# Optimization experiments

Hardware: AMD Instinct MI355X
Metric: run time of the kernel (lower is better)

Reference implementation:

```python
import jax, jax.numpy as jnp
import numpy as np

K_SEM = 5          # max_semantic_edges
THRESH = 0.2       # semantic_threshold
NEG_INF = -1e30


def setup_inputs() -> dict:
    key = jax.random.key(0)
    k1, k2 = jax.random.split(key)
    message_embeddings = jax.random.normal(k1, (8192, 256), dtype=jnp.float32)
    edge_emb_table = jax.random.normal(k2, (2, 64), dtype=jnp.float32)
    return {"message_embeddings": message_embeddings, "edge_emb_table": edge_emb_table}


def reference(message_embeddings, edge_emb_table):
    N = message_embeddings.shape[0]

    # ---- temporal edges: for each i -> [i,i+1] then [i+1,i] (interleaved) ----
    i = jnp.arange(N - 1)
    fwd = jnp.stack([i, i + 1])            # [2, N-1]
    bwd = jnp.stack([i + 1, i])            # [2, N-1]
    temporal = jnp.stack([fwd, bwd], axis=2).reshape(2, -1)   # [2, 2(N-1)]
    n_temporal = 2 * (N - 1)

    # ---- semantic edges: per-row top-k over sim[i, :i] with threshold ----
    norm = jnp.sqrt(jnp.sum(message_embeddings * message_embeddings, axis=1, keepdims=True))
    emb_n = message_embeddings / jnp.maximum(norm, 1e-12)     # F.normalize(p=2)
    sim = emb_n @ emb_n.T                                      # [N, N]

    r = jnp.arange(N)[:, None]
    c = jnp.arange(N)[None, :]
    # zero out diagonal and adjacent (temporal) pairs, as the torch mask does
    sim = sim * (jnp.abs(r - c) > 1)
    # restrict candidates to j < i (strictly earlier messages)
    cand = jnp.where(c < r, sim, NEG_INF)                      # [N, N]

    vals, idxs = jax.lax.top_k(cand, K_SEM)                    # [N, K]
    sem_src = idxs.reshape(-1)                                 # [N*K]
    sem_dst = jnp.repeat(jnp.arange(N), K_SEM)                 # [N*K]
    sem_valid = (vals > THRESH).reshape(-1)                    # [N*K]

    # ---- assemble padded fixed-size edge set ----
    edge_index = jnp.concatenate([temporal, jnp.stack([sem_src, sem_dst])], axis=1)
    edge_types = jnp.concatenate(
        [jnp.zeros((n_temporal,), jnp.int32), jnp.ones((N * K_SEM,), jnp.int32)])
    valid = jnp.concatenate([jnp.ones((n_temporal,), bool), sem_valid])

    edge_attr = edge_emb_table[edge_types] * valid[:, None].astype(edge_emb_table.dtype)
    edge_index = jnp.where(valid[None, :], edge_index, -1)
    return edge_index, edge_attr, valid
```

## Files before the change

kernel.cpp:

```cpp
#include <hip/hip_runtime.h>

#define N_MSG 8192
#define DIM 256
#define KS 5
#define THRESH 0.2f
#define QSCALE 192.0f
#define FILT_I 6672
#define N_TEMPORAL (2*(N_MSG-1))
#define N_EDGES (N_TEMPORAL + N_MSG*KS)
#define ATTR_OFF (2*N_EDGES)
#define VALID_OFF (ATTR_OFF + N_EDGES*64)
#define BM 128
#define NTILE (N_MSG / BM)
#define NBLOCKS (NTILE*(NTILE+1)/2)
#define CAP 32

typedef int i32x4 __attribute__((ext_vector_type(4)));

__device__ __forceinline__ void ins5(float v, int j, float (&vv)[KS], int (&xx)[KS]) {
    float cv = v; int cj = j;
#pragma unroll
    for (int k = 0; k < KS; ++k) {
        bool b = (cv > vv[k]) || (cv == vv[k] && cj < xx[k]);
        float tv = b ? vv[k] : cv; int tj = b ? xx[k] : cj;
        vv[k] = b ? cv : vv[k];    xx[k] = b ? cj : xx[k];
        cv = tv; cj = tj;
    }
}

__global__ void normalize_k(const float* __restrict__ emb, float* __restrict__ embn,
                            unsigned int* __restrict__ embqT, int* __restrict__ cnt) {
    int lane = threadIdx.x & 63;
    int row = blockIdx.x * 4 + (threadIdx.x >> 6);
    const float4 x = *(const float4*)(emb + (size_t)row * DIM + lane * 4);
    float ss = x.x * x.x;
    ss = fmaf(x.y, x.y, ss); ss = fmaf(x.z, x.z, ss); ss = fmaf(x.w, x.w, ss);
#pragma unroll
    for (int off = 1; off <= 32; off <<= 1) ss += __shfl_xor(ss, off);
    float nrm = fmaxf(sqrtf(ss), 1e-12f);
    float4 y; y.x = x.x / nrm; y.y = x.y / nrm; y.z = x.z / nrm; y.w = x.w / nrm;
    *(float4*)(embn + (size_t)row * DIM + lane * 4) = y;
    int q0 = (int)rintf(fminf(fmaxf(y.x * QSCALE, -127.f), 127.f));
    int q1 = (int)rintf(fminf(fmaxf(y.y * QSCALE, -127.f), 127.f));
    int q2 = (int)rintf(fminf(fmaxf(y.z * QSCALE, -127.f), 127.f));
    int q3 = (int)rintf(fminf(fmaxf(y.w * QSCALE, -127.f), 127.f));
    unsigned int packed =
        (q0 & 255) | ((q1 & 255) << 8) | ((q2 & 255) << 16) | ((q3 & 255) << 24);
    embqT[(((size_t)(lane >> 2) * N_MSG + row) << 2) | (lane & 3)] = packed;
    if (lane == 0) cnt[row] = 0;
}

__global__ __launch_bounds__(256, 4)
void sim_filter_k(const i32x4* __restrict__ T, int* __restrict__ cnt,
                  int* __restrict__ cidx) {
    int t = blockIdx.x;
    int bi = (int)((sqrtf(8.0f * (float)t + 1.0f) - 1.0f) * 0.5f);
    while ((bi + 1) * (bi + 2) / 2 <= t) ++bi;
    while (bi * (bi + 1) / 2 > t) --bi;
    int bj = t - bi * (bi + 1) / 2;
    const int i0 = bi * BM, j0 = bj * BM;

    const int tid = threadIdx.x;
    const int lane = tid & 63;
    const int ws = tid >> 6;
    const int wm = ws >> 1, wn = ws & 1;
    const int lr = lane & 15, kb = lane >> 4;

    i32x4 acc[4][4];
#pragma unroll
    for (int m = 0; m < 4; ++m)
#pragma unroll
        for (int n = 0; n < 4; ++n) { i32x4 z = {0, 0, 0, 0}; acc[m][n] = z; }

#pragma unroll
    for (int kc = 0; kc < 4; ++kc) {
        const i32x4* Tc = T + (size_t)(kc * 4 + kb) * N_MSG;
        i32x4 a[4], b[4];
#pragma unroll
        for (int f = 0; f < 4; ++f) {
            a[f] = Tc[i0 + wm * 64 + f * 16 + lr];
            b[f] = Tc[j0 + wn * 64 + f * 16 + lr];
        }
#pragma unroll
        for (int m = 0; m < 4; ++m)
#pragma unroll
            for (int n = 0; n < 4; ++n)
                acc[m][n] = __builtin_amdgcn_mfma_i32_16x16x64_i8(a[m], b[n], acc[m][n], 0, 0, 0);
    }

#pragma unroll
    for (int m = 0; m < 4; ++m) {
        int i = i0 + wm * 64 + m * 16 + kb * 4;
#pragma unroll
        for (int n = 0; n < 4; ++n) {
            int j = j0 + wn * 64 + n * 16 + lr;
#pragma unroll
            for (int r = 0; r < 4; ++r) {
                int v = acc[m][n][r];
                int ii = i + r;
                if (v > FILT_I && j <= ii - 2) {
                    int c = atomicAdd(&cnt[ii], 1);
                    if (c < CAP) cidx[(size_t)ii * CAP + c] = j;
                }
            }
        }
    }
}

template<bool FUSE>
__global__ void rescue_k(const float* __restrict__ embn, const int* __restrict__ cnt,
                         const int* __restrict__ cidx, const float* __restrict__ table,
                         float* __restrict__ out) {
    int lane = threadIdx.x & 63;
    int i = blockIdx.x * 4 + (threadIdx.x >> 6);
    int nc = cnt[i]; if (nc > CAP) nc = CAP;

    float fv[KS]; int fx[KS];
#pragma unroll
    for (int k = 0; k < KS; ++k) { fv[k] = -1e30f; fx[k] = -1; }

    if (nc > 0) {
        const float4 a = *(const float4*)(embn + (size_t)i * DIM + lane * 4);
        for (int c = 0; c < nc; ++c) {
            int j = cidx[(size_t)i * CAP + c];
            const float4 b = *(const float4*)(embn + (size_t)j * DIM + lane * 4);
            float p = a.x * b.x;
            p = fmaf(a.y, b.y, p); p = fmaf(a.z, b.z, p); p = fmaf(a.w, b.w, p);
#pragma unroll
            for (int off = 1; off <= 32; off <<= 1) p += __shfl_xor(p, off);
            if (p > THRESH) ins5(p, j, fv, fx);
        }
    }
    int vcnt = 0;
#pragma unroll
    for (int k = 0; k < KS; ++k) vcnt += (fv[k] > THRESH) ? 1 : 0;

    float tsem = FUSE ? table[64 + lane] : 0.0f;
#pragma unroll
    for (int k = 0; k < KS; ++k) {
        int e = N_TEMPORAL + i * KS + k;
        bool val = (k < vcnt);
        if (lane == 0) {
            out[e]             = val ? (float)fx[k] : -1.0f;
            out[N_EDGES + e]   = val ? (float)i     : -1.0f;
            out[VALID_OFF + e] = val ? 1.0f : 0.0f;
        }
        if (FUSE) out[ATTR_OFF + (size_t)e * 64 + lane] = val ? tsem : 0.0f;
    }
    if (FUSE) {
        if (i < N_MSG - 1) {
            float ttem = table[lane];
            int e0 = 2 * i;
            out[ATTR_OFF + (size_t)e0 * 64 + lane]       = ttem;
            out[ATTR_OFF + (size_t)(e0 + 1) * 64 + lane] = ttem;
            if (lane == 0) {
                out[e0]                 = (float)i;
                out[N_EDGES + e0]       = (float)(i + 1);
                out[VALID_OFF + e0]     = 1.0f;
                out[e0 + 1]             = (float)(i + 1);
                out[N_EDGES + e0 + 1]   = (float)i;
                out[VALID_OFF + e0 + 1] = 1.0f;
            }
        }
    }
}

__global__ void attr_out_k(const float* __restrict__ table, float* __restrict__ out) {
    int idx = blockIdx.x * 256 + threadIdx.x;
    int e = idx >> 4, sub = idx & 15;
    if (e >= N_EDGES) return;
    float4 a4;
    if (e < N_TEMPORAL) {
        a4 = *(const float4*)(table + sub * 4);
        if (sub == 0) {
            int i = e >> 1;
            out[e]             = (e & 1) ? (float)(i + 1) : (float)i;
            out[N_EDGES + e]   = (e & 1) ? (float)i       : (float)(i + 1);
            out[VALID_OFF + e] = 1.0f;
        }
    } else {
        float vld = out[VALID_OFF + e];
        a4 = *(const float4*)(table + 64 + sub * 4);
        a4.x *= vld; a4.y *= vld; a4.z *= vld; a4.w *= vld;
    }
    *(float4*)(out + ATTR_OFF + (size_t)e * 64 + sub * 4) = a4;
}

extern "C" void kernel_launch(void* const* d_in, const int* in_sizes, int n_in,
                              void* d_out, int out_size, void* d_ws, size_t ws_size,
                              hipStream_t stream) {
    const float* emb   = (const float*)d_in[0];
    const float* table = (const float*)d_in[1];
    float* out = (float*)d_out;

    size_t embn_f  = (size_t)N_MSG * DIM;
    size_t embq_f  = (size_t)N_MSG * DIM / 4;
    size_t cidx_f  = (size_t)N_MSG * CAP;
    size_t cnt_f   = N_MSG;
    size_t need_bytes = (embn_f + embq_f + cidx_f + cnt_f) * 4;

    bool have_ws = (ws_size >= need_bytes);
    float* scratch = have_ws ? (float*)d_ws
                             : out + ATTR_OFF;
    float*        embn  = scratch;
    unsigned int* embqT = (unsigned int*)(scratch + embn_f);
    int*          cidx  = (int*)(scratch + embn_f + embq_f);
    int*          cnt   = (int*)(scratch + embn_f + embq_f + cidx_f);

    normalize_k<<<N_MSG / 4, 256, 0, stream>>>(emb, embn, embqT, cnt);
    sim_filter_k<<<NBLOCKS, 256, 0, stream>>>((const i32x4*)embqT, cnt, cidx);
    if (have_ws) {
        rescue_k<true><<<N_MSG / 4, 256, 0, stream>>>(embn, cnt, cidx, table, out);
    } else {
        rescue_k<false><<<N_MSG / 4, 256, 0, stream>>>(embn, cnt, cidx, table, out);
        attr_out_k<<<((size_t)N_EDGES * 16 + 255) / 256, 256, 0, stream>>>(table, out);
    }
}
```

Measured before the change: 62.83 us.

## Fuse three stages into one persistent kernel with software grid barriers

Replaces the normalize, int8 similarity filter and rescue launches with a single persistent kernel of 768 blocks. The stages are separated by atomic-counter grid barriers, which removes launch gaps between them. The MFMA loop also double-buffers its K-chunk register loads so loads overlap compute. The cost is a memset launch, barrier spin time, and a deadlock risk if all 768 blocks cannot be co-resident.

After: 196.6 us. +212.9%, slower.

```diff
diff --git a/kernel.cpp b/kernel.cpp
--- a/kernel.cpp
+++ b/kernel.cpp
@@ -14,6 +14,7 @@
 #define NTILE (N_MSG / BM)
 #define NBLOCKS (NTILE*(NTILE+1)/2)
 #define CAP 32
+#define GRID_F 768
 
 typedef int i32x4 __attribute__((ext_vector_type(4)));
 
@@ -25,6 +26,177 @@
         float tv = b ? vv[k] : cv; int tj = b ? xx[k] : cj;
         vv[k] = b ? cv : vv[k];    xx[k] = b ? cj : xx[k];
         cv = tv; cj = tj;
+    }
+}
+
+__device__ __forceinline__ void grid_bar(int* bars, int which) {
+    __syncthreads();
+    if (threadIdx.x == 0) {
+        int* base = bars + which * 128;
+        __threadfence();
+        atomicAdd(base + (blockIdx.x & 7) * 16, 1);
+        int s;
+        do {
+            s = 0;
+#pragma unroll
+            for (int q = 0; q < 8; ++q)
+                s += __hip_atomic_load(base + q * 16, __ATOMIC_RELAXED,
+                                       __HIP_MEMORY_SCOPE_AGENT);
+            if (s < GRID_F) __builtin_amdgcn_s_sleep(2);
+        } while (s < GRID_F);
+        __threadfence();
+    }
+    __syncthreads();
+}
+
+__global__ __launch_bounds__(256, 3)
+void fused_k(const float* __restrict__ emb, const float* __restrict__ table,
+             float* __restrict__ out, float* __restrict__ embn,
+             unsigned int* __restrict__ embqT, int* __restrict__ cnt,
+             int* __restrict__ cidx, int* __restrict__ gbar) {
+    const int tid = threadIdx.x;
+    const int bid = blockIdx.x;
+    const int lane = tid & 63;
+    const int wv = tid >> 6;
+
+    for (int g = bid; g < N_MSG / 4; g += GRID_F) {
+        int row = g * 4 + wv;
+        const float4 x = *(const float4*)(emb + (size_t)row * DIM + lane * 4);
+        float ss = x.x * x.x;
+        ss = fmaf(x.y, x.y, ss); ss = fmaf(x.z, x.z, ss); ss = fmaf(x.w, x.w, ss);
+#pragma unroll
+        for (int off = 1; off <= 32; off <<= 1) ss += __shfl_xor(ss, off);
+        float nrm = fmaxf(sqrtf(ss), 1e-12f);
+        float4 y; y.x = x.x / nrm; y.y = x.y / nrm; y.z = x.z / nrm; y.w = x.w / nrm;
+        *(float4*)(embn + (size_t)row * DIM + lane * 4) = y;
+        int q0 = (int)rintf(fminf(fmaxf(y.x * QSCALE, -127.f), 127.f));
+        int q1 = (int)rintf(fminf(fmaxf(y.y * QSCALE, -127.f), 127.f));
+        int q2 = (int)rintf(fminf(fmaxf(y.z * QSCALE, -127.f), 127.f));
+        int q3 = (int)rintf(fminf(fmaxf(y.w * QSCALE, -127.f), 127.f));
+        unsigned int packed =
+            (q0 & 255) | ((q1 & 255) << 8) | ((q2 & 255) << 16) | ((q3 & 255) << 24);
+        embqT[(((size_t)(lane >> 2) * N_MSG + row) << 2) | (lane & 3)] = packed;
+        if (lane == 0) cnt[row] = 0;
+    }
+    grid_bar(gbar, 0);
+
+    {
+        const i32x4* T = (const i32x4*)embqT;
+        const int ws = tid >> 6;
+        const int wm = ws >> 1, wn = ws & 1;
+        const int lr = lane & 15, kb = lane >> 4;
+
+        for (int t = bid; t < NBLOCKS; t += GRID_F) {
+            int bi = (int)((sqrtf(8.0f * (float)t + 1.0f) - 1.0f) * 0.5f);
+            while ((bi + 1) * (bi + 2) / 2 <= t) ++bi;
+            while (bi * (bi + 1) / 2 > t) --bi;
+            int bj = t - bi * (bi + 1) / 2;
+            const int i0 = bi * BM, j0 = bj * BM;
+
+            i32x4 acc[4][4];
+#pragma unroll
+            for (int m = 0; m < 4; ++m)
+#pragma unroll
+                for (int n = 0; n < 4; ++n) { i32x4 z = {0, 0, 0, 0}; acc[m][n] = z; }
+
+            auto LD = [&](int kc, i32x4* a, i32x4* b) {
+                const i32x4* Tc = T + (size_t)((kc << 2) + kb) * N_MSG;
+#pragma unroll
+                for (int f = 0; f < 4; ++f) {
+                    a[f] = Tc[i0 + wm * 64 + f * 16 + lr];
+                    b[f] = Tc[j0 + wn * 64 + f * 16 + lr];
+                }
+            };
+            auto COMP = [&](i32x4* a, i32x4* b) {
+#pragma unroll
+                for (int m = 0; m < 4; ++m)
+#pragma unroll
+                    for (int n = 0; n < 4; ++n)
+                        acc[m][n] = __builtin_amdgcn_mfma_i32_16x16x64_i8(
+                            a[m], b[n], acc[m][n], 0, 0, 0);
+            };
+
+            i32x4 a0[4], b0[4], a1[4], b1[4];
+            LD(0, a0, b0);
+            LD(1, a1, b1);
+            COMP(a0, b0);
+            LD(2, a0, b0);
+            COMP(a1, b1);
+            LD(3, a1, b1);
+            COMP(a0, b0);
+            COMP(a1, b1);
+
+#pragma unroll
+            for (int m = 0; m < 4; ++m) {
+                int i = i0 + wm * 64 + m * 16 + kb * 4;
+#pragma unroll
+                for (int n = 0; n < 4; ++n) {
+                    int j = j0 + wn * 64 + n * 16 + lr;
+#pragma unroll
+                    for (int r = 0; r < 4; ++r) {
+                        int v = acc[m][n][r];
+                        int ii = i + r;
+                        if (v > FILT_I && j <= ii - 2) {
+                            int c = atomicAdd(&cnt[ii], 1);
+                            if (c < CAP) cidx[(size_t)ii * CAP + c] = j;
+                        }
+                    }
+                }
+            }
+        }
+    }
+    grid_bar(gbar, 1);
+
+    for (int g = bid; g < N_MSG / 4; g += GRID_F) {
+        int i = g * 4 + wv;
+        int nc = cnt[i]; if (nc > CAP) nc = CAP;
+
+        float fv[KS]; int fx[KS];
+#pragma unroll
+        for (int k = 0; k < KS; ++k) { fv[k] = -1e30f; fx[k] = -1; }
+
+        if (nc > 0) {
+            const float4 a = *(const float4*)(embn + (size_t)i * DIM + lane * 4);
+            for (int c = 0; c < nc; ++c) {
+                int j = cidx[(size_t)i * CAP + c];
+                const float4 b = *(const float4*)(embn + (size_t)j * DIM + lane * 4);
+                float p = a.x * b.x;
+                p = fmaf(a.y, b.y, p); p = fmaf(a.z, b.z, p); p = fmaf(a.w, b.w, p);
+#pragma unroll
+                for (int off = 1; off <= 32; off <<= 1) p += __shfl_xor(p, off);
+                if (p > THRESH) ins5(p, j, fv, fx);
+            }
+        }
+        int vcnt = 0;
+#pragma unroll
+        for (int k = 0; k < KS; ++k) vcnt += (fv[k] > THRESH) ? 1 : 0;
+
+        float tsem = table[64 + lane];
+#pragma unroll
+        for (int k = 0; k < KS; ++k) {
+            int e = N_TEMPORAL + i * KS + k;
+            bool val = (k < vcnt);
+            if (lane == 0) {
+                out[e]             = val ? (float)fx[k] : -1.0f;
+                out[N_EDGES + e]   = val ? (float)i     : -1.0f;
+                out[VALID_OFF + e] = val ? 1.0f : 0.0f;
+            }
+            out[ATTR_OFF + (size_t)e * 64 + lane] = val ? tsem : 0.0f;
+        }
+        if (i < N_MSG - 1) {
+            float ttem = table[lane];
+            int e0 = 2 * i;
+            out[ATTR_OFF + (size_t)e0 * 64 + lane]       = ttem;
+            out[ATTR_OFF + (size_t)(e0 + 1) * 64 + lane] = ttem;
+            if (lane == 0) {
+                out[e0]                 = (float)i;
+                out[N_EDGES + e0]       = (float)(i + 1);
+                out[VALID_OFF + e0]     = 1.0f;
+                out[e0 + 1]             = (float)(i + 1);
+                out[N_EDGES + e0 + 1]   = (float)i;
+                out[VALID_OFF + e0 + 1] = 1.0f;
+            }
+        }
     }
 }
 
@@ -59,7 +231,6 @@
     while (bi * (bi + 1) / 2 > t) --bi;
     int bj = t - bi * (bi + 1) / 2;
     const int i0 = bi * BM, j0 = bj * BM;
-
     const int tid = threadIdx.x;
     const int lane = tid & 63;
     const int ws = tid >> 6;
@@ -71,7 +242,6 @@
     for (int m = 0; m < 4; ++m)
 #pragma unroll
         for (int n = 0; n < 4; ++n) { i32x4 z = {0, 0, 0, 0}; acc[m][n] = z; }
-
 #pragma unroll
     for (int kc = 0; kc < 4; ++kc) {
         const i32x4* Tc = T + (size_t)(kc * 4 + kb) * N_MSG;
@@ -87,7 +257,6 @@
             for (int n = 0; n < 4; ++n)
                 acc[m][n] = __builtin_amdgcn_mfma_i32_16x16x64_i8(a[m], b[n], acc[m][n], 0, 0, 0);
     }
-
 #pragma unroll
     for (int m = 0; m < 4; ++m) {
         int i = i0 + wm * 64 + m * 16 + kb * 4;
@@ -107,18 +276,14 @@
     }
 }
 
-template<bool FUSE>
-__global__ void rescue_k(const float* __restrict__ embn, const int* __restrict__ cnt,
-                         const int* __restrict__ cidx, const float* __restrict__ table,
-                         float* __restrict__ out) {
+__global__ void rescue_nf_k(const float* __restrict__ embn, const int* __restrict__ cnt,
+                            const int* __restrict__ cidx, float* __restrict__ out) {
     int lane = threadIdx.x & 63;
     int i = blockIdx.x * 4 + (threadIdx.x >> 6);
     int nc = cnt[i]; if (nc > CAP) nc = CAP;
-
     float fv[KS]; int fx[KS];
 #pragma unroll
     for (int k = 0; k < KS; ++k) { fv[k] = -1e30f; fx[k] = -1; }
-
     if (nc > 0) {
         const float4 a = *(const float4*)(embn + (size_t)i * DIM + lane * 4);
         for (int c = 0; c < nc; ++c) {
@@ -134,34 +299,12 @@
     int vcnt = 0;
 #pragma unroll
     for (int k = 0; k < KS; ++k) vcnt += (fv[k] > THRESH) ? 1 : 0;
-
-    float tsem = FUSE ? table[64 + lane] : 0.0f;
-#pragma unroll
-    for (int k = 0; k < KS; ++k) {
-        int e = N_TEMPORAL + i * KS + k;
-        bool val = (k < vcnt);
-        if (lane == 0) {
-            out[e]             = val ? (float)fx[k] : -1.0f;
-            out[N_EDGES + e]   = val ? (float)i     : -1.0f;
-            out[VALID_OFF + e] = val ? 1.0f : 0.0f;
-        }
-        if (FUSE) out[ATTR_OFF + (size_t)e * 64 + lane] = val ? tsem : 0.0f;
-    }
-    if (FUSE) {
-        if (i < N_MSG - 1) {
-            float ttem = table[lane];
-            int e0 = 2 * i;
-            out[ATTR_OFF + (size_t)e0 * 64 + lane]       = ttem;
-            out[ATTR_OFF + (size_t)(e0 + 1) * 64 + lane] = ttem;
-            if (lane == 0) {
-                out[e0]                 = (float)i;
-                out[N_EDGES + e0]       = (float)(i + 1);
-                out[VALID_OFF + e0]     = 1.0f;
-                out[e0 + 1]             = (float)(i + 1);
-                out[N_EDGES + e0 + 1]   = (float)i;
-                out[VALID_OFF + e0 + 1] = 1.0f;
-            }
-        }
+    if (lane < KS) {
+        int e = N_TEMPORAL + i * KS + lane;
+        bool val = (lane < vcnt);
+        out[e]             = val ? (float)fx[lane] : -1.0f;
+        out[N_EDGES + e]   = val ? (float)i        : -1.0f;
+        out[VALID_OFF + e] = val ? 1.0f : 0.0f;
     }
 }
 
@@ -197,7 +340,8 @@
     size_t embq_f  = (size_t)N_MSG * DIM / 4;
     size_t cidx_f  = (size_t)N_MSG * CAP;
     size_t cnt_f   = N_MSG;
-    size_t need_bytes = (embn_f + embq_f + cidx_f + cnt_f) * 4;
+    size_t gbar_f  = 256;
+    size_t need_bytes = (embn_f + embq_f + cidx_f + cnt_f + gbar_f) * 4;
 
     bool have_ws = (ws_size >= need_bytes);
     float* scratch = have_ws ? (float*)d_ws
@@ -206,13 +350,15 @@
     unsigned int* embqT = (unsigned int*)(scratch + embn_f);
     int*          cidx  = (int*)(scratch + embn_f + embq_f);
     int*          cnt   = (int*)(scratch + embn_f + embq_f + cidx_f);
-
-    normalize_k<<<N_MSG / 4, 256, 0, stream>>>(emb, embn, embqT, cnt);
-    sim_filter_k<<<NBLOCKS, 256, 0, stream>>>((const i32x4*)embqT, cnt, cidx);
+    int*          gbar  = (int*)(scratch + embn_f + embq_f + cidx_f + cnt_f);
+
     if (have_ws) {
-        rescue_k<true><<<N_MSG / 4, 256, 0, stream>>>(embn, cnt, cidx, table, out);
+        hipMemsetAsync(gbar, 0, gbar_f * 4, stream);
+        fused_k<<<GRID_F, 256, 0, stream>>>(emb, table, out, embn, embqT, cnt, cidx, gbar);
     } else {
-        rescue_k<false><<<N_MSG / 4, 256, 0, stream>>>(embn, cnt, cidx, table, out);
+        normalize_k<<<N_MSG / 4, 256, 0, stream>>>(emb, embn, embqT, cnt);
+        sim_filter_k<<<NBLOCKS, 256, 0, stream>>>((const i32x4*)embqT, cnt, cidx);
+        rescue_nf_k<<<N_MSG / 4, 256, 0, stream>>>(embn, cnt, cidx, out);
         attr_out_k<<<((size_t)N_EDGES * 16 + 255) / 256, 256, 0, stream>>>(table, out);
     }
 }
```

## Double-buffer int8 MFMA operand loads and vectorize edge-attribute stores

Applied to the files above, without the earlier changes.

In the similarity filter kernel, the four k-chunks now load operands into two alternating register sets, so the next chunk's global loads are issued before the current chunk's MFMAs. Launch bounds drop from 4 to 3 blocks per SM to leave room for the extra registers. The rescue kernel writes the semantic and temporal edge-attribute rows as float4 stores spread across lanes, replacing per-lane scalar stores, and groups the scalar index and valid writes under lane 0. The trade-off is higher register pressure and lower occupancy in exchange for load latency hiding and wider, more coalesced stores.

Result: slower. 65.40 us (+4.1%).

```diff
diff --git a/kernel.cpp b/kernel.cpp
--- a/kernel.cpp
+++ b/kernel.cpp
@@ -50,7 +50,7 @@
     if (lane == 0) cnt[row] = 0;
 }
 
-__global__ __launch_bounds__(256, 4)
+__global__ __launch_bounds__(256, 3)
 void sim_filter_k(const i32x4* __restrict__ T, int* __restrict__ cnt,
                   int* __restrict__ cidx) {
     int t = blockIdx.x;
@@ -72,21 +72,32 @@
 #pragma unroll
         for (int n = 0; n < 4; ++n) { i32x4 z = {0, 0, 0, 0}; acc[m][n] = z; }
 
-#pragma unroll
-    for (int kc = 0; kc < 4; ++kc) {
-        const i32x4* Tc = T + (size_t)(kc * 4 + kb) * N_MSG;
-        i32x4 a[4], b[4];
+    auto LD = [&](int kc, i32x4* a, i32x4* b) {
+        const i32x4* Tc = T + (size_t)((kc << 2) + kb) * N_MSG;
 #pragma unroll
         for (int f = 0; f < 4; ++f) {
             a[f] = Tc[i0 + wm * 64 + f * 16 + lr];
             b[f] = Tc[j0 + wn * 64 + f * 16 + lr];
         }
+    };
+    auto COMP = [&](i32x4* a, i32x4* b) {
 #pragma unroll
         for (int m = 0; m < 4; ++m)
 #pragma unroll
             for (int n = 0; n < 4; ++n)
-                acc[m][n] = __builtin_amdgcn_mfma_i32_16x16x64_i8(a[m], b[n], acc[m][n], 0, 0, 0);
-    }
+                acc[m][n] = __builtin_amdgcn_mfma_i32_16x16x64_i8(
+                    a[m], b[n], acc[m][n], 0, 0, 0);
+    };
+
+    i32x4 a0[4], b0[4], a1[4], b1[4];
+    LD(0, a0, b0);
+    LD(1, a1, b1);
+    COMP(a0, b0);
+    LD(2, a0, b0);
+    COMP(a1, b1);
+    LD(3, a1, b1);
+    COMP(a0, b0);
+    COMP(a1, b1);
 
 #pragma unroll
     for (int m = 0; m < 4; ++m) {
@@ -135,32 +146,45 @@
 #pragma unroll
     for (int k = 0; k < KS; ++k) vcnt += (fv[k] > THRESH) ? 1 : 0;
 
-    float tsem = FUSE ? table[64 + lane] : 0.0f;
-#pragma unroll
-    for (int k = 0; k < KS; ++k) {
-        int e = N_TEMPORAL + i * KS + k;
-        bool val = (k < vcnt);
-        if (lane == 0) {
+    if (lane == 0) {
+#pragma unroll
+        for (int k = 0; k < KS; ++k) {
+            int e = N_TEMPORAL + i * KS + k;
+            bool val = (k < vcnt);
             out[e]             = val ? (float)fx[k] : -1.0f;
             out[N_EDGES + e]   = val ? (float)i     : -1.0f;
             out[VALID_OFF + e] = val ? 1.0f : 0.0f;
         }
-        if (FUSE) out[ATTR_OFF + (size_t)e * 64 + lane] = val ? tsem : 0.0f;
-    }
+        if (FUSE && i < N_MSG - 1) {
+            int e0 = 2 * i;
+            out[e0]                 = (float)i;
+            out[N_EDGES + e0]       = (float)(i + 1);
+            out[VALID_OFF + e0]     = 1.0f;
+            out[e0 + 1]             = (float)(i + 1);
+            out[N_EDGES + e0 + 1]   = (float)i;
+            out[VALID_OFF + e0 + 1] = 1.0f;
+        }
+    }
+
     if (FUSE) {
-        if (i < N_MSG - 1) {
-            float ttem = table[lane];
-            int e0 = 2 * i;
-            out[ATTR_OFF + (size_t)e0 * 64 + lane]       = ttem;
-            out[ATTR_OFF + (size_t)(e0 + 1) * 64 + lane] = ttem;
-            if (lane == 0) {
-                out[e0]                 = (float)i;
-                out[N_EDGES + e0]       = (float)(i + 1);
-                out[VALID_OFF + e0]     = 1.0f;
-                out[e0 + 1]             = (float)(i + 1);
-                out[N_EDGES + e0 + 1]   = (float)i;
-                out[VALID_OFF + e0 + 1] = 1.0f;
+#pragma unroll
+        for (int rep = 0; rep < 2; ++rep) {
+            int slot = rep * 64 + lane;
+            if (slot < KS * 16) {
+                int k = slot >> 4, sub = slot & 15;
+                int e = N_TEMPORAL + i * KS + k;
+                float4 t4 = *(const float4*)(table + 64 + sub * 4);
+                bool val = (k < vcnt);
+                float4 w; w.x = val ? t4.x : 0.f; w.y = val ? t4.y : 0.f;
+                w.z = val ? t4.z : 0.f; w.w = val ? t4.w : 0.f;
+                *(float4*)(out + ATTR_OFF + (size_t)e * 64 + sub * 4) = w;
             }
+        }
+        if (i < N_MSG - 1 && lane < 32) {
+            int k = lane >> 4, sub = lane & 15;
+            int e = 2 * i + k;
+            float4 t4 = *(const float4*)(table + sub * 4);
+            *(float4*)(out + ATTR_OFF + (size_t)e * 64 + sub * 4) = t4;
         }
     }
 }
```
